# Optimization experiments

Measured on AMD Instinct MI355X. Metric: run time of the kernel, lower is better.

The kernel has to match this reference:

```python
import jax, jax.numpy as jnp
import numpy as np

B, T, D = 4, 2048, 1024
C_BIAS = 0.0  # init kwarg c
LN_EPS = 1e-5


def setup_inputs() -> dict:
    key = jax.random.key(0)
    ks = jax.random.split(key, 8)
    s = 1.0 / np.sqrt(D)
    return {
        "x": jax.random.normal(ks[0], (B, T, D), dtype=jnp.float32),
        "l": jax.random.randint(ks[1], (B,), 1, T + 1),  # lengths in [1, T]
        "Wq": jax.random.normal(ks[2], (D, D), dtype=jnp.float32) * s,
        "Wk": jax.random.normal(ks[3], (D, D), dtype=jnp.float32) * s,
        "Wv": jax.random.normal(ks[4], (D, D), dtype=jnp.float32) * s,
        "Wo": jax.random.normal(ks[5], (D, D), dtype=jnp.float32) * s,
        "bo": jnp.zeros((D,), dtype=jnp.float32),
        "gamma": jnp.ones((D,), dtype=jnp.float32),
        "beta": jnp.zeros((D,), dtype=jnp.float32),
    }


def reference(x, l, Wq, Wk, Wv, Wo, bo, gamma, beta):
    # LayerNorm over last dim
    mu = jnp.mean(x, axis=-1, keepdims=True)
    var = jnp.mean(jnp.square(x - mu), axis=-1, keepdims=True)
    x_norm = (x - mu) * jax.lax.rsqrt(var + LN_EPS) * gamma + beta

    # QKV projections (torch Linear: y = x @ W.T, no bias)
    q = jnp.einsum("btd,ed->bte", x_norm, Wq)
    k = jnp.einsum("btd,ed->bte", x_norm, Wk)
    v = jnp.einsum("btd,ed->bte", x_norm, Wv)

    scale = 1.0 / jnp.sqrt(jnp.float32(D))
    scores = C_BIAS + jnp.einsum("bid,bjd->bij", q, k) * scale  # [B,T,T]

    # Mask is applied along the ROW (dim 1) axis, and softmax is over dim 1
    # (faithful to the original: mask.unsqueeze(2) + Softmax(dim=1)).
    valid_rows = jnp.arange(T)[None, :] < l[:, None]  # [B,T]
    scores = jnp.where(valid_rows[:, :, None], scores, -jnp.inf)
    attn = jax.nn.softmax(scores, axis=1)  # normalize over rows

    y = x + jnp.einsum("bij,bjd->bid", attn, v)
    out = jax.nn.relu(jnp.einsum("btd,ed->bte", y, Wo) + bo)
    return out
```

## Files before the change

### kernel.cpp

```cpp
#include <hip/hip_runtime.h>
#include <hip/hip_fp16.h>

typedef unsigned short u16;
typedef __attribute__((ext_vector_type(8))) short bf16x8;
typedef __attribute__((ext_vector_type(4))) float f32x4;

#define T_SEQ 2048
#define DIM 1024
#define NB 4
#define NCH 8

__device__ __forceinline__ u16 f2bf(float f) {
  union { float f; unsigned u; } c; c.f = f;
  unsigned r = c.u + 0x7fffu + ((c.u >> 16) & 1u);
  return (u16)(r >> 16);
}

__device__ __forceinline__ void gload_lds16(const void* g, void* l) {
  __builtin_amdgcn_global_load_lds((const __attribute__((address_space(1))) void*)g,
                                   (__attribute__((address_space(3))) void*)l, 16, 0, 0);
}

#define SBAR() asm volatile("s_barrier" ::: "memory")
#define WVL(n) asm volatile("s_waitcnt vmcnt(" n ") lgkmcnt(0)" ::: "memory")
#define VMC(n) asm volatile("s_waitcnt vmcnt(" n ")" ::: "memory")

__global__ __launch_bounds__(256) void ln_kernel(const float* __restrict__ x,
                                                 const float* __restrict__ gamma,
                                                 const float* __restrict__ beta,
                                                 u16* __restrict__ xn) {
  const int row = blockIdx.x;
  const int tid = threadIdx.x;
  const float4 v = *(const float4*)(x + (size_t)row * DIM + tid * 4);
  float s  = v.x + v.y + v.z + v.w;
  float ss = v.x * v.x + v.y * v.y + v.z * v.z + v.w * v.w;
#pragma unroll
  for (int o = 32; o > 0; o >>= 1) { s += __shfl_down(s, o); ss += __shfl_down(ss, o); }
  __shared__ float rs[4], rss[4];
  const int wid = tid >> 6, lane = tid & 63;
  if (lane == 0) { rs[wid] = s; rss[wid] = ss; }
  __syncthreads();
  s  = rs[0] + rs[1] + rs[2] + rs[3];
  ss = rss[0] + rss[1] + rss[2] + rss[3];
  const float mu = s * (1.f / DIM);
  const float var = ss * (1.f / DIM) - mu * mu;
  const float rstd = rsqrtf(var + 1e-5f);
  const float4 g  = *(const float4*)(gamma + tid * 4);
  const float4 be = *(const float4*)(beta + tid * 4);
  ushort4 o;
  o.x = f2bf((v.x - mu) * rstd * g.x + be.x);
  o.y = f2bf((v.y - mu) * rstd * g.y + be.y);
  o.z = f2bf((v.z - mu) * rstd * g.z + be.z);
  o.w = f2bf((v.w - mu) * rstd * g.w + be.w);
  *(ushort4*)(xn + (size_t)row * DIM + tid * 4) = o;
}

__global__ __launch_bounds__(256) void wcvt4(const float* __restrict__ wq,
                                             const float* __restrict__ wk,
                                             const float* __restrict__ wv,
                                             const float* __restrict__ wo,
                                             u16* __restrict__ dqk,
                                             u16* __restrict__ dv,
                                             u16* __restrict__ dw) {
  const int sel = blockIdx.x >> 10;
  const size_t t = (size_t)(blockIdx.x & 1023) * 256 + threadIdx.x;
  const float* w = (sel == 0) ? wq : (sel == 1) ? wk : (sel == 2) ? wv : wo;
  u16* d = (sel == 0) ? dqk : (sel == 1) ? (dqk + 1048576) : (sel == 2) ? dv : dw;
  const float4 v = *(const float4*)(w + t * 4);
  ushort4 u; u.x = f2bf(v.x); u.y = f2bf(v.y); u.z = f2bf(v.z); u.w = f2bf(v.w);
  *(ushort4*)(d + t * 4) = u;
}

template <int EPI, int MSK>
__global__ __launch_bounds__(512, 2) void gemm8(
    const u16* __restrict__ A, const u16* __restrict__ B, void* __restrict__ Cv,
    int K, int lda, int ldb, int ldc,
    long sA, long sB, long sC, float scale,
    const int* __restrict__ lptr, float* __restrict__ mpQ, float* __restrict__ zpQ) {
  __shared__ __align__(16) u16 As[2][2][8192];
  __shared__ __align__(16) u16 Bs[2][2][8192];
  const int bz = blockIdx.z;
  const u16* Ab = A + (size_t)bz * sA;
  const u16* Bb = B + (size_t)bz * sB;

  const int nb = gridDim.x * gridDim.y;
  int bid = blockIdx.y * gridDim.x + blockIdx.x;
  bid = (bid & 7) * (nb >> 3) + (bid >> 3);
  const int gx = gridDim.x;
  const int tileN = (bid % gx) * 256;
  const int tileM = (bid / gx) * 256;

  if constexpr (MSK == 1) {
    if (tileM >= lptr[bz]) return;
  }
  if constexpr (MSK == 3) {
    if (((tileM & (T_SEQ - 1)) >= lptr[tileM >> 11]) && tileN < DIM) return;
  }

  const int t = threadIdx.x;
  const int lane = t & 63;
  const int wid = t >> 6;
  const int wm = wid >> 2, wn = wid & 3;

  const int srow = wid * 32 + (lane >> 2);
  const int schk = ((t & 3) ^ (srow & 3) ^ ((srow >> 2) & 3)) * 8;
  const size_t aof = (size_t)(tileM + srow) * lda + schk;
  const size_t bof = (size_t)(tileN + srow) * ldb + schk;
  const size_t a16 = 16 * (size_t)lda, b16 = 16 * (size_t)ldb;
  const int dst0 = wid * 1024 + lane * 8;

  const int frow = lane & 15, kg = lane >> 4;
  const int rsw = (kg ^ (frow & 3) ^ ((frow >> 2) & 3)) * 8;
  const int arow = wm * 128 + frow;
  const int brow = wn * 64 + frow;

#define STG_A(bf, kk, tg) do { \
    const size_t _s = aof + (size_t)(tg) * 64 + (kk) * 32; \
    gload_lds16(Ab + _s, &As[bf][kk][dst0]); \
    gload_lds16(Ab + _s + a16, &As[bf][kk][dst0 + 512]); } while (0)
#define STG_B(bf, kk, tg) do { \
    const size_t _s = bof + (size_t)(tg) * 64 + (kk) * 32; \
    gload_lds16(Bb + _s, &Bs[bf][kk][dst0]); \
    gload_lds16(Bb + _s + b16, &Bs[bf][kk][dst0 + 512]); } while (0)
#define LDA4(bf, kk, h, AF) do { \
    _Pragma("unroll") for (int _i = 0; _i < 4; ++_i) \
      AF[_i] = *(const bf16x8*)&As[bf][kk][(arow + (h) * 64 + _i * 16) * 32 + rsw]; } while (0)
#define LDB4(bf, kk, BF) do { \
    _Pragma("unroll") for (int _j = 0; _j < 4; ++_j) \
      BF[_j] = *(const bf16x8*)&Bs[bf][kk][(brow + _j * 16) * 32 + rsw]; } while (0)
#define MFM(h, AF, BF) do { __builtin_amdgcn_s_setprio(1); \
    _Pragma("unroll") for (int _i = 0; _i < 4; ++_i) \
      _Pragma("unroll") for (int _j = 0; _j < 4; ++_j) \
        acc[(h) * 4 + _i][_j] = __builtin_amdgcn_mfma_f32_16x16x32_bf16( \
            AF[_i], BF[_j], acc[(h) * 4 + _i][_j], 0, 0, 0); \
    __builtin_amdgcn_s_setprio(0); } while (0)

  f32x4 acc[8][4] = {};
  const int NT = K >> 6;

  STG_B(0, 0, 0); STG_A(0, 0, 0);
  STG_B(0, 1, 0); STG_A(0, 1, 0);
  STG_B(1, 0, 1); STG_A(1, 0, 1);
  VMC("4");
  SBAR();

  for (int tt = 0; tt < NT; tt += 2) {
    const bool st = (tt + 2 < NT);
    bf16x8 af[4], bq0[4], bq1[4];
    LDA4(0, 0, 0, af); LDB4(0, 0, bq0);
    STG_B(1, 1, tt + 1);
    SBAR(); MFM(0, af, bq0);
    LDA4(0, 0, 1, af);
    STG_A(1, 1, tt + 1);
    SBAR(); MFM(1, af, bq0);
    LDA4(0, 1, 0, af); LDB4(0, 1, bq1);
    if (st) STG_B(0, 0, tt + 2);
    SBAR(); MFM(0, af, bq1);
    LDA4(0, 1, 1, af);
    if (st) { STG_A(0, 0, tt + 2); VMC("4"); } else { VMC("0"); }
    SBAR(); MFM(1, af, bq1);
    LDA4(1, 0, 0, af); LDB4(1, 0, bq0);
    if (st) STG_B(0, 1, tt + 2);
    SBAR(); MFM(0, af, bq0);
    LDA4(1, 0, 1, af);
    if (st) STG_A(0, 1, tt + 2);
    SBAR(); MFM(1, af, bq0);
    LDA4(1, 1, 0, af); LDB4(1, 1, bq1);
    if (st) STG_B(1, 0, tt + 3);
    SBAR(); MFM(0, af, bq1);
    LDA4(1, 1, 1, af);
    if (st) { STG_A(1, 0, tt + 3); VMC("2"); } else { VMC("0"); }
    SBAR(); MFM(1, af, bq1);
  }
#undef STG_A
#undef STG_B
#undef LDA4
#undef LDB4
#undef MFM

  const int r0 = tileM + wm * 128 + (kg << 2);
  const int c0 = tileN + wn * 64 + frow;
#pragma unroll
  for (int i = 0; i < 8; ++i)
#pragma unroll
    for (int j = 0; j < 4; ++j)
#pragma unroll
      for (int r = 0; r < 4; ++r) {
        const int row = r0 + i * 16 + r, col = c0 + j * 16;
        const size_t idx = (size_t)row * ldc + col;
        const float v = acc[i][j][r];
        if constexpr (EPI == 0) {
          ((u16*)Cv + (size_t)bz * sC)[idx] = f2bf(v);
        } else {
          ((__half*)Cv + (size_t)bz * sC)[idx] = __float2half(v * scale);
        }
      }

  if constexpr (EPI == 1) {
    const int L = lptr[bz];
    __shared__ float2 red[2][4][4][16];
    float Ms[4], Zs[4];
#pragma unroll
    for (int j = 0; j < 4; ++j) {
      float mj = -3e38f;
#pragma unroll
      for (int i = 0; i < 8; ++i)
#pragma unroll
        for (int r = 0; r < 4; ++r) {
          const int row = r0 + i * 16 + r;
          if (row < L) mj = fmaxf(mj, acc[i][j][r] * scale);
        }
      mj = fmaxf(mj, __shfl_xor(mj, 16, 64));
      mj = fmaxf(mj, __shfl_xor(mj, 32, 64));
      float zj = 0.f;
#pragma unroll
      for (int i = 0; i < 8; ++i)
#pragma unroll
        for (int r = 0; r < 4; ++r) {
          const int row = r0 + i * 16 + r;
          if (row < L) zj += __expf(acc[i][j][r] * scale - mj);
        }
      zj += __shfl_xor(zj, 16, 64);
      zj += __shfl_xor(zj, 32, 64);
      Ms[j] = mj; Zs[j] = zj;
    }
    if (lane < 16) {
#pragma unroll
      for (int j = 0; j < 4; ++j) red[wm][wn][j][frow] = make_float2(Ms[j], Zs[j]);
    }
    __syncthreads();
    if (wm == 0 && lane < 16) {
#pragma unroll
      for (int j = 0; j < 4; ++j) {
        const float2 a = red[0][wn][j][frow];
        const float2 b = red[1][wn][j][frow];
        const float M = fmaxf(a.x, b.x);
        const float Z = a.y * __expf(a.x - M) + b.y * __expf(b.x - M);
        const int col = tileN + wn * 64 + j * 16 + frow;
        const size_t o = ((size_t)(tileM >> 8) * NB + bz) * T_SEQ + col;
        mpQ[o] = M; zpQ[o] = Z;
      }
    }
  }
}

template <int EPI, int MSK>
__global__ __launch_bounds__(512, 2) void gemm_bt(
    const u16* __restrict__ A, const u16* __restrict__ B, void* __restrict__ Cv,
    int K, int lda, int ldb, int ldc,
    long sA, long sB, long sC,
    const float* __restrict__ aux, long sAux,
    const int* __restrict__ lptr) {
  __shared__ __align__(16) u16 As[4][128 * 32];
  __shared__ __align__(16) u16 Bs[4][256 * 32];
  const int bz = blockIdx.z;
  const u16* Ab = A + (size_t)bz * sA;
  const u16* Bb = B + (size_t)bz * sB;

  const int nb = gridDim.x * gridDim.y;
  int bid = blockIdx.y * gridDim.x + blockIdx.x;
  bid = (bid & 7) * (nb >> 3) + (bid >> 3);
  const int gx = gridDim.x;
  const int tileN = (bid % gx) * 256;
  const int tileM = (bid / gx) * 128;

  const int t = threadIdx.x;

  if constexpr (MSK == 2) {
    if (tileM >= lptr[bz]) {
      const float* xb = aux + (size_t)bz * sAux;
      u16* yo = (u16*)Cv + (size_t)bz * sC;
      for (int e = t; e < (128 * 256) / 8; e += 512) {
        const int row = tileM + (e >> 5);
        const int col = tileN + ((e & 31) << 3);
        const float4 v0 = *(const float4*)(xb + (size_t)row * ldc + col);
        const float4 v1 = *(const float4*)(xb + (size_t)row * ldc + col + 4);
        ushort4 o0; o0.x = f2bf(v0.x); o0.y = f2bf(v0.y); o0.z = f2bf(v0.z); o0.w = f2bf(v0.w);
        ushort4 o1; o1.x = f2bf(v1.x); o1.y = f2bf(v1.y); o1.z = f2bf(v1.z); o1.w = f2bf(v1.w);
        *(ushort4*)(yo + (size_t)row * ldc + col) = o0;
        *(ushort4*)(yo + (size_t)row * ldc + col + 4) = o1;
      }
      return;
    }
  }

  const int lane = t & 63;
  const int wid = t >> 6;
  const int wm = wid >> 2, wn = wid & 3;

  const int srow = t >> 2;
  const int qsw = (((t & 3) ^ (srow & 3) ^ ((srow >> 2) & 3))) * 8;
  const size_t aoff0 = (size_t)(tileM + srow) * lda + qsw;
  const size_t boff0 = (size_t)(tileN + srow) * ldb + qsw;
  const size_t boff1 = (size_t)(tileN + 128 + srow) * ldb + qsw;

  const int frow = lane & 15;
  const int kg = lane >> 4;
  const int ckk = ((kg ^ (lane & 3) ^ ((lane >> 2) & 3))) * 8;

  f32x4 acc[4][4] = {};
  const int NT = K >> 5;

#pragma unroll
  for (int p = 0; p < 3; ++p) {
    const size_t kp = (size_t)p << 5;
    gload_lds16(Ab + aoff0 + kp, &As[p][t * 8]);
    gload_lds16(Bb + boff0 + kp, &Bs[p][t * 8]);
    gload_lds16(Bb + boff1 + kp, &Bs[p][4096 + t * 8]);
  }
  VMC("6");
  SBAR();

  for (int tau = 0; tau < NT; ++tau) {
    const int cur = tau & 3;
    const int tgt = (tau + 3) & 3;
    const bool st = (tau + 3 < NT);
    const size_t k0 = (size_t)(tau + 3) << 5;

    bf16x8 af[4], bf[4];
#pragma unroll
    for (int j = 0; j < 4; ++j)
      bf[j] = *(const bf16x8*)&Bs[cur][(wn * 64 + j * 16 + frow) * 32 + ckk];
#pragma unroll
    for (int i = 0; i < 4; ++i)
      af[i] = *(const bf16x8*)&As[cur][(wm * 64 + i * 16 + frow) * 32 + ckk];
    if (st) {
      gload_lds16(Ab + aoff0 + k0, &As[tgt][t * 8]);
      gload_lds16(Bb + boff0 + k0, &Bs[tgt][t * 8]);
      gload_lds16(Bb + boff1 + k0, &Bs[tgt][4096 + t * 8]);
    }
    if (tau < NT - 3) WVL("6"); else if (tau == NT - 3) WVL("3"); else WVL("0");
    SBAR();
    __builtin_amdgcn_s_setprio(1);
#pragma unroll
    for (int i = 0; i < 4; ++i)
#pragma unroll
      for (int j = 0; j < 4; ++j)
        acc[i][j] = __builtin_amdgcn_mfma_f32_16x16x32_bf16(af[i], bf[j], acc[i][j], 0, 0, 0);
    __builtin_amdgcn_s_setprio(0);
  }

  const int r0 = tileM + wm * 64 + (kg << 2);
  const int c0 = tileN + wn * 64 + frow;
#pragma unroll
  for (int i = 0; i < 4; ++i)
#pragma unroll
    for (int j = 0; j < 4; ++j)
#pragma unroll
      for (int r = 0; r < 4; ++r) {
        const int row = r0 + i * 16 + r, col = c0 + j * 16;
        const size_t idx = (size_t)row * ldc + col;
        float v = acc[i][j][r];
        if constexpr (EPI == 0) {
          ((u16*)Cv + (size_t)bz * sC)[idx] = f2bf(v);
        } else if constexpr (EPI == 2) {
          v += (aux + (size_t)bz * sAux)[idx];
          ((u16*)Cv + (size_t)bz * sC)[idx] = f2bf(v);
        } else {
          v += aux[col];
          ((float*)Cv + (size_t)bz * sC)[idx] = fmaxf(v, 0.f);
        }
      }
}

__global__ __launch_bounds__(256) void colreduce_comb(const float* __restrict__ mp,
                                                      const float* __restrict__ zp,
                                                      const int* __restrict__ l,
                                                      float* __restrict__ m,
                                                      float* __restrict__ rz) {
  const int b = blockIdx.y;
  const int j = blockIdx.x * 256 + threadIdx.x;
  const int L = l[b];
  float M = -3e38f, Z = 0.f;
  for (int c = 0; c < NCH && (c << 8) < L; ++c) {
    const size_t o = ((size_t)c * NB + b) * T_SEQ + j;
    const float mc = mp[o], zc = zp[o];
    const float nm = fmaxf(M, mc);
    Z = Z * __expf(M - nm) + zc * __expf(mc - nm);
    M = nm;
  }
  m[b * T_SEQ + j] = M;
  rz[b * T_SEQ + j] = 1.f / Z;
}

__global__ __launch_bounds__(256) void pbuild(const __half* __restrict__ S,
                                              const int* __restrict__ l,
                                              const float* __restrict__ m,
                                              const float* __restrict__ rz,
                                              u16* __restrict__ P) {
  const int b = blockIdx.x >> 11;
  const int i = blockIdx.x & (T_SEQ - 1);
  const int L = l[b];
  if (i >= ((L + 127) & ~127)) return;
  const int j0 = threadIdx.x * 8;
  const size_t off = ((size_t)blockIdx.x << 11) + j0;
  ushort4 o0, o1;
  if (i < L) {
    const __half* sp = S + off;
    const float* mp = m + b * T_SEQ + j0;
    const float* zp = rz + b * T_SEQ + j0;
    u16 tmp[8];
#pragma unroll
    for (int tt = 0; tt < 8; ++tt)
      tmp[tt] = f2bf(__expf(__half2float(sp[tt]) - mp[tt]) * zp[tt]);
    o0 = make_ushort4(tmp[0], tmp[1], tmp[2], tmp[3]);
    o1 = make_ushort4(tmp[4], tmp[5], tmp[6], tmp[7]);
  } else {
    o0 = make_ushort4(0, 0, 0, 0);
    o1 = make_ushort4(0, 0, 0, 0);
  }
  *(ushort4*)(P + off) = o0;
  *(ushort4*)(P + off + 4) = o1;
}

extern "C" void kernel_launch(void* const* d_in, const int* in_sizes, int n_in,
                              void* d_out, int out_size, void* d_ws, size_t ws_size,
                              hipStream_t stream) {
  (void)in_sizes; (void)n_in; (void)out_size; (void)ws_size;
  const float* x     = (const float*)d_in[0];
  const int*   l     = (const int*)d_in[1];
  const float* Wq    = (const float*)d_in[2];
  const float* Wk    = (const float*)d_in[3];
  const float* Wv    = (const float*)d_in[4];
  const float* Wo    = (const float*)d_in[5];
  const float* bo    = (const float*)d_in[6];
  const float* gamma = (const float*)d_in[7];
  const float* beta  = (const float*)d_in[8];

  char* ws = (char*)d_ws;
  const size_t MiB = 1024 * 1024;
  u16* xn   = (u16*)(ws);
  u16* wqkb = (u16*)(ws + 16 * MiB);
  u16* wvb  = (u16*)(ws + 20 * MiB);
  u16* wob  = (u16*)(ws + 22 * MiB);
  u16* QKb  = (u16*)(ws + 24 * MiB);
  u16* Vt   = (u16*)(ws + 56 * MiB);
  float* mpart = (float*)(ws + 20 * MiB);
  float* zpart = (float*)(ws + 20 * MiB + 512 * 1024);
  float* mb  = (float*)(ws + 72 * MiB);
  float* rzb = (float*)(ws + 72 * MiB + 32 * 1024);
  u16* Pb = QKb;
  u16* yb = xn;
  __half* S = (__half*)d_out;
  float* outp = (float*)d_out;

  const long TD = (long)T_SEQ * DIM, TT = (long)T_SEQ * T_SEQ;
  const long TQK = (long)T_SEQ * 2048;

  ln_kernel<<<NB * T_SEQ, 256, 0, stream>>>(x, gamma, beta, xn);
  wcvt4<<<4096, 256, 0, stream>>>(Wq, Wk, Wv, Wo, wqkb, wvb, wob);

  gemm8<0, 3><<<dim3(8, 32, 1), 512, 0, stream>>>(
      xn, wqkb, QKb, DIM, DIM, DIM, 2048, 0, 0, 0, 0.f, l, nullptr, nullptr);
  gemm_bt<0, 0><<<dim3(32, 8, 1), 512, 0, stream>>>(
      wvb, xn, Vt, DIM, DIM, DIM, 8192, 0, 0, 0, nullptr, 0, nullptr);
  gemm8<1, 1><<<dim3(8, 8, NB), 512, 0, stream>>>(
      QKb, QKb + 1024, S, DIM, 2048, 2048, T_SEQ, TQK, TQK, TT, 0.03125f,
      l, mpart, zpart);
  colreduce_comb<<<dim3(T_SEQ / 256, NB), 256, 0, stream>>>(mpart, zpart, l, mb, rzb);
  pbuild<<<NB * T_SEQ, 256, 0, stream>>>(S, l, mb, rzb, Pb);
  gemm_bt<2, 2><<<dim3(4, 16, NB), 512, 0, stream>>>(
      Pb, Vt, yb, T_SEQ, T_SEQ, 8192, DIM, TT, 2048, TD, x, TD, l);
  gemm_bt<3, 0><<<dim3(4, 64, 1), 512, 0, stream>>>(
      yb, wob, outp, DIM, DIM, DIM, DIM, 0, 0, 0, bo, 0, nullptr);
}
```

Measured before the change: 208.7 us.

## Restructure GEMM LDS layout to 64-wide K rows with 8-way XOR swizzle and quadrant pipeline

Changes the shared-memory staging layout from two 32-wide K halves per buffer to full 64-wide K rows split by M/N halves, using an 8-way XOR swizzle. The main loop is rescheduled into quadrant-based MFMA phases that keep A fragments across two B quadrants and interleave global-to-LDS loads differently. The aim is fewer LDS bank conflicts and better overlap of loads with MFMAs. It adds extra barriers around each MFMA phase and uses more fragment registers.

```diff
diff --git a/kernel.cpp b/kernel.cpp
--- a/kernel.cpp
+++ b/kernel.cpp
@@ -102,80 +102,77 @@
   const int wid = t >> 6;
   const int wm = wid >> 2, wn = wid & 3;
 
-  const int srow = wid * 32 + (lane >> 2);
-  const int schk = ((t & 3) ^ (srow & 3) ^ ((srow >> 2) & 3)) * 8;
+  const int srow = t >> 3;
+  const int schk = ((t & 7) ^ (srow & 7)) * 8;
   const size_t aof = (size_t)(tileM + srow) * lda + schk;
   const size_t bof = (size_t)(tileN + srow) * ldb + schk;
-  const size_t a16 = 16 * (size_t)lda, b16 = 16 * (size_t)ldb;
-  const int dst0 = wid * 1024 + lane * 8;
 
   const int frow = lane & 15, kg = lane >> 4;
-  const int rsw = (kg ^ (frow & 3) ^ ((frow >> 2) & 3)) * 8;
-  const int arow = wm * 128 + frow;
-  const int brow = wn * 64 + frow;
-
-#define STG_A(bf, kk, tg) do { \
-    const size_t _s = aof + (size_t)(tg) * 64 + (kk) * 32; \
-    gload_lds16(Ab + _s, &As[bf][kk][dst0]); \
-    gload_lds16(Ab + _s + a16, &As[bf][kk][dst0 + 512]); } while (0)
-#define STG_B(bf, kk, tg) do { \
-    const size_t _s = bof + (size_t)(tg) * 64 + (kk) * 32; \
-    gload_lds16(Bb + _s, &Bs[bf][kk][dst0]); \
-    gload_lds16(Bb + _s + b16, &Bs[bf][kk][dst0 + 512]); } while (0)
-#define LDA4(bf, kk, h, AF) do { \
-    _Pragma("unroll") for (int _i = 0; _i < 4; ++_i) \
-      AF[_i] = *(const bf16x8*)&As[bf][kk][(arow + (h) * 64 + _i * 16) * 32 + rsw]; } while (0)
-#define LDB4(bf, kk, BF) do { \
-    _Pragma("unroll") for (int _j = 0; _j < 4; ++_j) \
-      BF[_j] = *(const bf16x8*)&Bs[bf][kk][(brow + _j * 16) * 32 + rsw]; } while (0)
-#define MFM(h, AF, BF) do { __builtin_amdgcn_s_setprio(1); \
-    _Pragma("unroll") for (int _i = 0; _i < 4; ++_i) \
-      _Pragma("unroll") for (int _j = 0; _j < 4; ++_j) \
-        acc[(h) * 4 + _i][_j] = __builtin_amdgcn_mfma_f32_16x16x32_bf16( \
-            AF[_i], BF[_j], acc[(h) * 4 + _i][_j], 0, 0, 0); \
-    __builtin_amdgcn_s_setprio(0); } while (0)
-
+  const int fr7 = frow & 7;
+
+  bf16x8 af[4][2], bq0[2][2], bq1[2][2];
   f32x4 acc[8][4] = {};
   const int NT = K >> 6;
 
-  STG_B(0, 0, 0); STG_A(0, 0, 0);
-  STG_B(0, 1, 0); STG_A(0, 1, 0);
-  STG_B(1, 0, 1); STG_A(1, 0, 1);
-  VMC("4");
+#define STG_A(bf, mh, tg) do { \
+    const u16* _s = Ab + aof + (size_t)(mh) * 128 * lda + (size_t)(tg) * 64; \
+    gload_lds16(_s, &As[bf][mh][t * 8]); \
+    gload_lds16(_s + 64 * (size_t)lda, &As[bf][mh][4096 + t * 8]); } while (0)
+#define STG_B(bf, nh, tg) do { \
+    const u16* _s = Bb + bof + (size_t)(nh) * 128 * ldb + (size_t)(tg) * 64; \
+    gload_lds16(_s, &Bs[bf][nh][t * 8]); \
+    gload_lds16(_s + 64 * (size_t)ldb, &Bs[bf][nh][4096 + t * 8]); } while (0)
+#define LDA(bf, qa) do { \
+    _Pragma("unroll") for (int _i = 0; _i < 4; ++_i) \
+    _Pragma("unroll") for (int _k = 0; _k < 2; ++_k) \
+      af[_i][_k] = *(const bf16x8*)&As[bf][wm][ \
+          (((qa) * 64 + _i * 16 + frow) << 6) + (((_k * 4 + kg) ^ fr7) << 3)]; } while (0)
+#define LDB(bf, qb, BQ) do { \
+    _Pragma("unroll") for (int _j = 0; _j < 2; ++_j) \
+    _Pragma("unroll") for (int _k = 0; _k < 2; ++_k) \
+      BQ[_j][_k] = *(const bf16x8*)&Bs[bf][wn >> 1][ \
+          ((((wn & 1) * 64 + (qb) * 32 + _j * 16 + frow)) << 6) + (((_k * 4 + kg) ^ fr7) << 3)]; } while (0)
+#define MFM(qa, qb, BQ) do { __builtin_amdgcn_s_setprio(1); \
+    _Pragma("unroll") for (int _k = 0; _k < 2; ++_k) \
+    _Pragma("unroll") for (int _i = 0; _i < 4; ++_i) \
+    _Pragma("unroll") for (int _j = 0; _j < 2; ++_j) \
+      acc[(qa) * 4 + _i][(qb) * 2 + _j] = __builtin_amdgcn_mfma_f32_16x16x32_bf16( \
+          af[_i][_k], BQ[_j][_k], acc[(qa) * 4 + _i][(qb) * 2 + _j], 0, 0, 0); \
+    __builtin_amdgcn_s_setprio(0); } while (0)
+
+  STG_B(0, 0, 0); STG_B(0, 1, 0); STG_A(0, 0, 0); STG_A(0, 1, 0);
+  STG_B(1, 0, 1); STG_B(1, 1, 1); STG_A(1, 0, 1);
+  VMC("6");
   SBAR();
 
-  for (int tt = 0; tt < NT; tt += 2) {
-    const bool st = (tt + 2 < NT);
-    bf16x8 af[4], bq0[4], bq1[4];
-    LDA4(0, 0, 0, af); LDB4(0, 0, bq0);
-    STG_B(1, 1, tt + 1);
-    SBAR(); MFM(0, af, bq0);
-    LDA4(0, 0, 1, af);
-    STG_A(1, 1, tt + 1);
-    SBAR(); MFM(1, af, bq0);
-    LDA4(0, 1, 0, af); LDB4(0, 1, bq1);
-    if (st) STG_B(0, 0, tt + 2);
-    SBAR(); MFM(0, af, bq1);
-    LDA4(0, 1, 1, af);
-    if (st) { STG_A(0, 0, tt + 2); VMC("4"); } else { VMC("0"); }
-    SBAR(); MFM(1, af, bq1);
-    LDA4(1, 0, 0, af); LDB4(1, 0, bq0);
-    if (st) STG_B(0, 1, tt + 2);
-    SBAR(); MFM(0, af, bq0);
-    LDA4(1, 0, 1, af);
-    if (st) STG_A(0, 1, tt + 2);
-    SBAR(); MFM(1, af, bq0);
-    LDA4(1, 1, 0, af); LDB4(1, 1, bq1);
-    if (st) STG_B(1, 0, tt + 3);
-    SBAR(); MFM(0, af, bq1);
-    LDA4(1, 1, 1, af);
-    if (st) { STG_A(1, 0, tt + 3); VMC("2"); } else { VMC("0"); }
-    SBAR(); MFM(1, af, bq1);
+  for (int n = 0; n < (NT >> 1); ++n) {
+    const int t1 = 2 * n + 1, t2 = 2 * n + 2, t3 = 2 * n + 3;
+    const bool st = (t2 < NT);
+    LDA(0, 0); LDB(0, 0, bq0);
+    STG_A(1, 1, t1);
+    SBAR(); MFM(0, 0, bq0); SBAR();
+    LDB(0, 1, bq1);
+    SBAR(); MFM(0, 1, bq1); SBAR();
+    LDA(0, 1);
+    if (st) { STG_B(0, 0, t2); STG_B(0, 1, t2); }
+    SBAR(); MFM(1, 0, bq0); SBAR();
+    if (st) { STG_A(0, 0, t2); VMC("6"); } else { VMC("0"); }
+    SBAR(); MFM(1, 1, bq1); SBAR();
+    LDA(1, 0); LDB(1, 0, bq0);
+    if (st) STG_A(0, 1, t2);
+    SBAR(); MFM(0, 0, bq0); SBAR();
+    LDB(1, 1, bq1);
+    SBAR(); MFM(0, 1, bq1); SBAR();
+    LDA(1, 1);
+    if (st) { STG_B(1, 0, t3); STG_B(1, 1, t3); }
+    SBAR(); MFM(1, 0, bq0); SBAR();
+    if (st) { STG_A(1, 0, t3); VMC("6"); } else { VMC("0"); }
+    SBAR(); MFM(1, 1, bq1); SBAR();
   }
 #undef STG_A
 #undef STG_B
-#undef LDA4
-#undef LDB4
+#undef LDA
+#undef LDB
 #undef MFM
 
   const int r0 = tileM + wm * 128 + (kg << 2);
```

After: 211.7 us. No clear change (+1.4%).
